# Optimization experiments

Measured on AMD Instinct MI355X. Metric: run time of the kernel, lower is better.

Reference implementation:

```python
import jax, jax.numpy as jnp
import numpy as np

B, L, E, H, W = 2, 8192, 1024, 16, 128
HD = E // H  # 64


def setup_inputs() -> dict:
    key = jax.random.key(0)
    ks = jax.random.split(key, 9)
    s = 1.0 / np.sqrt(E)
    inp = {"x": jax.random.normal(ks[0], (B, L, E), jnp.float32)}
    for i, n in enumerate(["Wq", "Wk", "Wv", "Wo"]):
        inp[n] = jax.random.uniform(ks[1 + i], (E, E), jnp.float32, -s, s)
    for i, n in enumerate(["bq", "bk", "bv", "bo"]):
        inp[n] = jax.random.uniform(ks[5 + i], (E,), jnp.float32, -s, s)
    return inp


def _skew_prob(p, w):
    # (..., w, 2w+1) -> (..., w, 3w) with row i right-shifted by i:
    # out[..., i, i+j] = p[..., i, j]  (zeros elsewhere)
    lead = p.shape[:-2]
    M, Lc = p.shape[-2], p.shape[-1]
    p = jnp.pad(p, [(0, 0)] * len(lead) + [(0, 0), (0, M + 1)])
    p = p.reshape(*lead, M * (Lc + M + 1))[..., :-M].reshape(*lead, M, M + Lc)
    return p[..., :-1]


def _sliding_attend(q, k, v, w):
    # q,k,v: (b,h,l,d); banded attention, window w on each side (2w+1 diagonals)
    b, h, l, d = q.shape
    c = l // w
    qc = q.reshape(b, h, c, w, d)
    # per-chunk key/value windows of 3w tokens (w halo each side, zero padded)
    idx = jnp.arange(c)[:, None] * w + jnp.arange(3 * w)[None, :]  # (c, 3w)
    kw = jnp.pad(k, ((0, 0), (0, 0), (w, w), (0, 0)))[:, :, idx]  # (b,h,c,3w,d)
    s = jnp.einsum('bhcqd,bhckd->bhcqk', qc, kw)  # (b,h,c,w,3w)
    # extract band: band[i, j] = s[i, i+j], j in [0, 2w] (offset d = j - w)
    gidx = (jnp.arange(w)[:, None] + jnp.arange(2 * w + 1)[None, :])[None, None, None]
    band = jnp.take_along_axis(s, gidx, axis=-1).reshape(b, h, l, 2 * w + 1)
    # mask out-of-range positions (matches the module's edge -inf loop)
    pos = jnp.arange(l)[:, None] + (jnp.arange(2 * w + 1) - w)[None, :]
    band = jnp.where((pos >= 0) & (pos < l), band, -jnp.inf)
    prob = jax.nn.softmax(band / np.sqrt(d), axis=-1)  # scale by sqrt(head_dim)
    vw = jnp.pad(v, ((0, 0), (0, 0), (w, w), (0, 0)))[:, :, idx]  # (b,h,c,3w,d)
    p3 = _skew_prob(prob.reshape(b, h, c, w, 2 * w + 1), w)  # (b,h,c,w,3w)
    ctx = jnp.einsum('bhcqk,bhckd->bhcqd', p3, vw)
    return ctx.reshape(b, h, l, d)


def reference(x, Wq, Wk, Wv, Wo, bq, bk, bv, bo):
    q = (x @ Wq.T + bq).reshape(B, L, H, HD).transpose(0, 2, 1, 3)
    k = (x @ Wk.T + bk).reshape(B, L, H, HD).transpose(0, 2, 1, 3)
    v = (x @ Wv.T + bv).reshape(B, L, H, HD).transpose(0, 2, 1, 3)
    ctx = _sliding_attend(q, k, v, W)
    ctx = ctx.transpose(0, 2, 1, 3).reshape(B, L, E)
    return ctx @ Wo.T + bo
```

## Files before the change

kernel.cpp:

```cpp
#include <hip/hip_runtime.h>
#include <math.h>

#define B_SZ  2
#define L_SEQ 8192
#define EMB   1024
#define NH    16
#define HDIM  64
#define WIN   128
#define MROWS (B_SZ*L_SEQ)

typedef __attribute__((ext_vector_type(8))) _Float16 f16x8;
typedef __attribute__((ext_vector_type(4))) _Float16 f16x4;
typedef __attribute__((ext_vector_type(4))) float f32x4;

__device__ __forceinline__ void gload16(const void* g, void* l) {
    __builtin_amdgcn_global_load_lds(
        (const __attribute__((address_space(1))) unsigned int*)g,
        (__attribute__((address_space(3))) unsigned int*)l, 16, 0, 0);
}

__global__ __launch_bounds__(256)
void round_all(const float* __restrict__ x,
               const float* __restrict__ wq, const float* __restrict__ wk,
               const float* __restrict__ wv, const float* __restrict__ wo,
               _Float16* __restrict__ xf, _Float16* __restrict__ q16,
               _Float16* __restrict__ k16, _Float16* __restrict__ v16,
               _Float16* __restrict__ o16)
{
    const size_t NX = (size_t)MROWS * EMB, NW = (size_t)EMB * EMB;
    size_t gid = ((size_t)blockIdx.x * 256 + threadIdx.x) * 4;
    const float* src; _Float16* dst; size_t off;
    if (gid < NX)               { src = x;  dst = xf;  off = gid; }
    else if (gid < NX + NW)     { src = wq; dst = q16; off = gid - NX; }
    else if (gid < NX + 2*NW)   { src = wk; dst = k16; off = gid - NX - 2*NW + NW; }
    else if (gid < NX + 3*NW)   { src = wv; dst = v16; off = gid - NX - 2*NW; }
    else                        { src = wo; dst = o16; off = gid - NX - 3*NW; }
    float4 v = *(const float4*)(src + off);
    f16x4 o;
    o[0] = (_Float16)v.x; o[1] = (_Float16)v.y;
    o[2] = (_Float16)v.z; o[3] = (_Float16)v.w;
    *(f16x4*)(dst + off) = o;
}


#define STAGE_HT(ptr_, tb_, op_, h_, kt_)                                      \
    {                                                                          \
        char* d_ = smem + (op_) * 65536 + ((kt_) & 1) * 32768 + (h_) * 16384 + ldst; \
        const _Float16* s_ = (ptr_) + ((size_t)((tb_) + (h_) * 128 + srow6)) * 1024 + (kt_) * 64 + gch; \
        gload16(s_, d_);                                                       \
        gload16(s_ + 64 * 1024, d_ + 8192);                                    \
    }

#define DSREAD_A(qr_)                                                          \
    _Pragma("unroll")                                                          \
    for (int i_ = 0; i_ < 4; ++i_) {                                           \
        const int ro_ = (qr_) * 8192 + (i_ * 16 + frow) * 128;                 \
        af[i_][0] = *(const f16x8*)(Ab + ro_ + sb0);                           \
        af[i_][1] = *(const f16x8*)(Ab + ro_ + sb1);                           \
    }

#define DSREAD_B(qc_)                                                          \
    _Pragma("unroll")                                                          \
    for (int j_ = 0; j_ < 2; ++j_) {                                           \
        const int ro_ = (brow + (qc_) * 32 + j_ * 16 + frow) * 128;            \
        bf[j_][0] = *(const f16x8*)(Bb + ro_ + sb0);                           \
        bf[j_][1] = *(const f16x8*)(Bb + ro_ + sb1);                           \
    }

#define MFMA16(qr_, qc_)                                                       \
    __builtin_amdgcn_s_setprio(1);                                             \
    _Pragma("unroll")                                                          \
    for (int ks_ = 0; ks_ < 2; ++ks_)                                          \
        _Pragma("unroll")                                                      \
        for (int i_ = 0; i_ < 4; ++i_)                                         \
            _Pragma("unroll")                                                  \
            for (int j_ = 0; j_ < 2; ++j_)                                     \
                acc[(qr_) * 4 + i_][(qc_) * 2 + j_] =                          \
                    __builtin_amdgcn_mfma_f32_16x16x32_f16(                    \
                        af[i_][ks_], bf[j_][ks_],                              \
                        acc[(qr_) * 4 + i_][(qc_) * 2 + j_], 0, 0, 0);         \
    __builtin_amdgcn_s_setprio(0);

#define BARM()                                                                 \
    asm volatile("" ::: "memory");                                             \
    __builtin_amdgcn_s_barrier();                                              \
    asm volatile("" ::: "memory");

#define GEMM8_CORE(Aptr, Bptr)                                                 \
    const int t = threadIdx.x;                                                 \
    const int wave = t >> 6, lane = t & 63;                                    \
    const int wr = wave >> 2, wc = wave & 3;                                   \
    const int frow = lane & 15, quad = lane >> 4;                              \
    const int srow6 = t >> 3;                                                  \
    const int gch = ((t & 7) ^ (srow6 & 7)) * 8;                               \
    const int ldst = t * 16;                                                   \
    const int sb0 = (quad ^ (frow & 7)) * 16, sb1 = sb0 ^ 64;                  \
    const int brow = (wc & 1) * 64;                                            \
    f32x4 acc[8][4] = {};                                                      \
    f16x8 af[4][2], bf[2][2];                                                  \
    STAGE_HT(Aptr, bm, 0, 0, 0) STAGE_HT(Aptr, bm, 0, 1, 0)                    \
    STAGE_HT(Bptr, bn, 1, 0, 0) STAGE_HT(Bptr, bn, 1, 1, 0)                    \
    for (int kt = 0; kt < 16; ++kt) {                                          \
        const char* Ab = smem + (kt & 1) * 32768 + wr * 16384;                 \
        const char* Bb = smem + 65536 + (kt & 1) * 32768 + (wc >> 1) * 16384;  \
        if (kt < 15) {                                                         \
            STAGE_HT(Aptr, bm, 0, 0, kt + 1)                                   \
            asm volatile("s_waitcnt vmcnt(2)" ::: "memory");                   \
        } else {                                                               \
            asm volatile("s_waitcnt vmcnt(0)" ::: "memory");                   \
        }                                                                      \
        BARM()                                                                 \
        DSREAD_A(0) DSREAD_B(0)                  \
        MFMA16(0, 0)                                                           \
        DSREAD_B(1)                            \
        if (kt < 15) STAGE_HT(Aptr, bm, 0, 1, kt + 1)                          \
        BARM()                                                                 \
        MFMA16(0, 1)                                                           \
        DSREAD_A(1)                                                            \
        if (kt < 15) STAGE_HT(Bptr, bn, 1, 0, kt + 1)                          \
        BARM()                                                                 \
        MFMA16(1, 1)                                                           \
        DSREAD_B(0)                                \
        if (kt < 15) STAGE_HT(Bptr, bn, 1, 1, kt + 1)                          \
        BARM()                                                                 \
        MFMA16(1, 0)                                                           \
        BARM()                                                                 \
    }

__global__ __launch_bounds__(512, 2)
void gemm_qkv(const _Float16* __restrict__ X,
              const _Float16* __restrict__ Wq, const _Float16* __restrict__ Wk,
              const _Float16* __restrict__ Wv,
              const float* __restrict__ bq, const float* __restrict__ bk,
              const float* __restrict__ bv,
              _Float16* __restrict__ qf, _Float16* __restrict__ kf,
              _Float16* __restrict__ vtf)
{
    __shared__ __attribute__((aligned(16))) char smem[131072];

    const int id = blockIdx.x;
    const int row = (id / 96) * 8 + (id & 7);
    const int colq = (id >> 3) % 12;
    const int wsel = colq >> 2;
    const int bm = row * 256, bn = (colq & 3) * 256;
    const _Float16* Bw = wsel == 0 ? Wq : wsel == 1 ? Wk : Wv;
    const float* bias = wsel == 0 ? bq : wsel == 1 ? bk : bv;
    const float scale = wsel == 0 ? 0.125f : 1.0f;

    GEMM8_CORE(X, Bw)

    char* Cw = smem + wave * 8192;
    const int bb = bm >> 13;
    const int l0 = (bm & (L_SEQ - 1)) + wr * 128;
    const int h = (bn >> 6) + wc;
    if (wsel < 2) {
        _Float16* dst = wsel == 0 ? qf : kf;
        const size_t hb = ((size_t)(bb * NH + h)) * L_SEQ * HDIM;
        #pragma unroll
        for (int ih = 0; ih < 2; ++ih) {
            asm volatile("" ::: "memory");
            #pragma unroll
            for (int i = 0; i < 4; ++i)
                #pragma unroll
                for (int j = 0; j < 4; ++j) {
                    const int lc = j * 16 + frow;
                    const float bvv = bias[bn + wc * 64 + lc];
                    #pragma unroll
                    for (int r = 0; r < 4; ++r) {
                        const int lr = i * 16 + quad * 4 + r;
                        const int bo = lr * 128 + ((lc * 2) ^ ((lr & 7) << 4));
                        *(_Float16*)(Cw + bo) = (_Float16)((acc[ih * 4 + i][j][r] + bvv) * scale);
                    }
                }
            asm volatile("" ::: "memory");
            #pragma unroll
            for (int p = 0; p < 8; ++p) {
                const int idx = p * 64 + lane;
                const int lr = idx >> 3, seg = idx & 7;
                const int bo = lr * 128 + ((seg * 16) ^ ((lr & 7) << 4));
                uint4 v = *(const uint4*)(Cw + bo);
                *(uint4*)&dst[hb + (size_t)(l0 + ih * 64 + lr) * HDIM + seg * 8] = v;
            }
        }
    } else {
        const size_t hb = ((size_t)(bb * NH + h)) * HDIM * L_SEQ;
        #pragma unroll
        for (int ih = 0; ih < 2; ++ih) {
            asm volatile("" ::: "memory");
            #pragma unroll
            for (int i = 0; i < 4; ++i)
                #pragma unroll
                for (int j = 0; j < 4; ++j) {
                    const int lc = j * 16 + frow;
                    const float bvv = bias[bn + wc * 64 + lc];
                    #pragma unroll
                    for (int r = 0; r < 4; ++r) {
                        const int lr = i * 16 + quad * 4 + r;
                        const int bo = lc * 128 + ((lr * 2) ^ ((lc & 7) << 4));
                        *(_Float16*)(Cw + bo) = (_Float16)(acc[ih * 4 + i][j][r] + bvv);
                    }
                }
            asm volatile("" ::: "memory");
            #pragma unroll
            for (int p = 0; p < 8; ++p) {
                const int idx = p * 64 + lane;
                const int dc = idx >> 3, sl = idx & 7;
                const int bo = dc * 128 + ((sl * 16) ^ ((dc & 7) << 4));
                uint4 v = *(const uint4*)(Cw + bo);
                *(uint4*)&vtf[hb + (size_t)dc * L_SEQ + (l0 + ih * 64 + sl * 8)] = v;
            }
        }
    }
}

__global__ __launch_bounds__(512, 2)
void gemm_out(const _Float16* __restrict__ A, const _Float16* __restrict__ Bwm,
              const float* __restrict__ bias, float* __restrict__ C)
{
    constexpr int N = EMB;
    __shared__ __attribute__((aligned(16))) char smem[131072];

    const int id = blockIdx.x;
    const int row = (id / 32) * 8 + (id & 7);
    const int bm = row * 256, bn = ((id >> 3) & 3) * 256;

    GEMM8_CORE(A, Bwm)

    #pragma unroll
    for (int i = 0; i < 8; ++i) {
        int m0 = bm + wr * 128 + i * 16 + quad * 4;
        #pragma unroll
        for (int j = 0; j < 4; ++j) {
            int n = bn + wc * 64 + j * 16 + frow;
            float bvv = bias[n];
            #pragma unroll
            for (int r = 0; r < 4; ++r)
                C[(size_t)(m0 + r) * N + n] = acc[i][j][r] + bvv;
        }
    }
}

__global__ __launch_bounds__(512)
void attn_mfma(const _Float16* __restrict__ qf, const _Float16* __restrict__ kf,
               const _Float16* __restrict__ vtf, _Float16* __restrict__ cf)
{
    __shared__ _Float16 Kf[2][4096], Vf[2][4096];

    const int t = threadIdx.x;
    const int wave = t >> 6, lane = t & 63;
    const int col = lane & 15, quad = lane >> 4;
    const int bh = blockIdx.y;
    const int q0 = blockIdx.x * 128;
    const int oo = wave * 16;

    f16x8 qfr[2];
    {
        size_t qidx = ((size_t)bh * L_SEQ + q0 + oo + col) * HDIM + quad * 8;
        qfr[0] = *(const f16x8*)(qf + qidx);
        qfr[1] = *(const f16x8*)(qf + qidx + 32);
    }

    f32x4 o[4] = {};
    float lsum = 0.0f;

    const int srow = t >> 3, sc = t & 7;

    const int ktlo = (q0 == 0) ? 2 : 0;
    const int kthi = (q0 == L_SEQ - 128) ? 4 : 6;

#define STAGE_KV(kt_, bsel_)                                                   \
    {                                                                          \
        const int p0s = q0 - WIN + (kt_) * 64;                                 \
        const int gq = sc ^ (srow & 7);                                        \
        size_t kgi = ((size_t)bh * L_SEQ + p0s + srow) * HDIM + gq * 8;        \
        size_t vgi = ((size_t)bh * HDIM + srow) * L_SEQ + p0s + gq * 8;        \
        gload16(kf + kgi, (char*)&Kf[bsel_][0] + t * 16);                      \
        gload16(vtf + vgi, (char*)&Vf[bsel_][0] + t * 16);                     \
    }

    STAGE_KV(ktlo, 0)

    for (int kt = ktlo; kt < kthi; kt++) {
        const int p0 = q0 - WIN + kt * 64;
        const int cb = (kt - ktlo) & 1;
        if (kt + 1 < kthi) {
            STAGE_KV(kt + 1, cb ^ 1)
            asm volatile("s_waitcnt vmcnt(2)" ::: "memory");
        } else {
            asm volatile("s_waitcnt vmcnt(0)" ::: "memory");
        }
        __builtin_amdgcn_s_barrier();
        asm volatile("" ::: "memory");

        const char* Kb = (const char*)&Kf[cb][0];
        const char* Vb = (const char*)&Vf[cb][0];

        const int relp = kt * 64 - WIN - oo;
        if (relp >= -191 && relp <= 143) {
            f32x4 sT[4] = {};
            #pragma unroll
            for (int ks = 0; ks < 2; ks++)
                #pragma unroll
                for (int n = 0; n < 4; n++) {
                    int off = (n * 16 + col) * 128 + (((ks * 4 + quad) ^ (col & 7)) * 16);
                    f16x8 kfr = *(const f16x8*)(Kb + off);
                    sT[n] = __builtin_amdgcn_mfma_f32_16x16x32_f16(kfr, qfr[ks], sT[n], 0, 0, 0);
                }
            if (relp < -113 || relp > 65) {
                const int qrow = q0 + oo + col;
                #pragma unroll
                for (int n = 0; n < 4; n++)
                    #pragma unroll
                    for (int r = 0; r < 4; r++) {
                        int dlt = (p0 + n * 16 + quad * 4 + r) - qrow;
                        if (dlt < -WIN || dlt > WIN) sT[n][r] = -3e38f;
                    }
            }
            f16x4 pT[4];
            #pragma unroll
            for (int n = 0; n < 4; n++)
                #pragma unroll
                for (int r = 0; r < 4; r++) {
                    float pv = __expf(sT[n][r]);
                    lsum += pv;
                    pT[n][r] = (_Float16)pv;
                }
            #pragma unroll
            for (int m = 0; m < 4; m++) {
                #pragma unroll
                for (int n = 0; n < 4; n++) {
                    int off = (m * 16 + col) * 128 +
                              (((2 * n + (quad >> 1)) ^ (col & 7)) * 16) + (quad & 1) * 8;
                    f16x4 vfr = *(const f16x4*)(Vb + off);
                    o[m] = __builtin_amdgcn_mfma_f32_16x16x16f16(vfr, pT[n], o[m], 0, 0, 0);
                }
            }
        }
        asm volatile("" ::: "memory");
        __builtin_amdgcn_s_barrier();
        asm volatile("" ::: "memory");
    }

    lsum += __shfl_xor(lsum, 16, 64);
    lsum += __shfl_xor(lsum, 32, 64);
    const float inv = 1.0f / lsum;

    const int b = bh >> 4, h = bh & 15;
    const size_t base = ((size_t)b * L_SEQ + q0 + oo + col) * EMB + h * HDIM;
    #pragma unroll
    for (int m = 0; m < 4; m++) {
        f16x4 ov;
        #pragma unroll
        for (int r = 0; r < 4; r++) ov[r] = (_Float16)(o[m][r] * inv);
        *(f16x4*)&cf[base + m * 16 + quad * 4] = ov;
    }
}

extern "C" void kernel_launch(void* const* d_in, const int* in_sizes, int n_in,
                              void* d_out, int out_size, void* d_ws, size_t ws_size,
                              hipStream_t stream) {
    const float* x  = (const float*)d_in[0];
    const float* Wq = (const float*)d_in[1];
    const float* Wk = (const float*)d_in[2];
    const float* Wv = (const float*)d_in[3];
    const float* Wo = (const float*)d_in[4];
    const float* bq = (const float*)d_in[5];
    const float* bk = (const float*)d_in[6];
    const float* bv = (const float*)d_in[7];
    const float* bo = (const float*)d_in[8];
    float* out = (float*)d_out;

    const size_t per = (size_t)B_SZ * NH * L_SEQ * HDIM;
    _Float16* w16 = (_Float16*)d_ws;
    _Float16* xf   = w16;
    _Float16* qf   = w16 + per;
    _Float16* kf   = w16 + 2 * per;
    _Float16* vtf  = w16 + 3 * per;
    _Float16* cf   = w16 + 4 * per;
    _Float16* wq16 = w16 + 5 * per;
    _Float16* wk16 = wq16 + 1048576;
    _Float16* wv16 = wq16 + 2 * 1048576;
    _Float16* wo16 = wq16 + 3 * 1048576;

    const int nround = (MROWS * EMB + 4 * EMB * EMB) / 1024;
    round_all<<<nround, dim3(256), 0, stream>>>(x, Wq, Wk, Wv, Wo, xf, wq16, wk16, wv16, wo16);

    gemm_qkv<<<768, dim3(512), 0, stream>>>(xf, wq16, wk16, wv16, bq, bk, bv, qf, kf, vtf);

    attn_mfma<<<dim3(L_SEQ / 128, B_SZ * NH), dim3(512), 0, stream>>>(qf, kf, vtf, cf);

    gemm_out<<<256, dim3(512), 0, stream>>>(cf, wo16, bo, out);
}
```

Before: 314.3 us.

## Restructure GEMM mainloop into unrolled double-buffered phases with deeper prefetch

```diff
diff --git a/kernel.cpp b/kernel.cpp
--- a/kernel.cpp
+++ b/kernel.cpp
@@ -51,20 +51,20 @@
         gload16(s_ + 64 * 1024, d_ + 8192);                                    \
     }
 
-#define DSREAD_A(qr_)                                                          \
+#define DSR_A(base_, qr_)                                                      \
     _Pragma("unroll")                                                          \
     for (int i_ = 0; i_ < 4; ++i_) {                                           \
-        const int ro_ = (qr_) * 8192 + (i_ * 16 + frow) * 128;                 \
-        af[i_][0] = *(const f16x8*)(Ab + ro_ + sb0);                           \
-        af[i_][1] = *(const f16x8*)(Ab + ro_ + sb1);                           \
-    }
-
-#define DSREAD_B(qc_)                                                          \
+        const int ro_ = ((qr_) * 64 + i_ * 16 + frow) * 128;                   \
+        af[i_][0] = *(const f16x8*)((base_) + ro_ + sb0);                      \
+        af[i_][1] = *(const f16x8*)((base_) + ro_ + sb1);                      \
+    }
+
+#define DSR_B(base_, qc_)                                                      \
     _Pragma("unroll")                                                          \
     for (int j_ = 0; j_ < 2; ++j_) {                                           \
         const int ro_ = (brow + (qc_) * 32 + j_ * 16 + frow) * 128;            \
-        bf[j_][0] = *(const f16x8*)(Bb + ro_ + sb0);                           \
-        bf[j_][1] = *(const f16x8*)(Bb + ro_ + sb1);                           \
+        bf[j_][0] = *(const f16x8*)((base_) + ro_ + sb0);                      \
+        bf[j_][1] = *(const f16x8*)((base_) + ro_ + sb1);                      \
     }
 
 #define MFMA16(qr_, qc_)                                                       \
@@ -86,6 +86,19 @@
     __builtin_amdgcn_s_barrier();                                              \
     asm volatile("" ::: "memory");
 
+#define VW4 asm volatile("s_waitcnt vmcnt(4)" ::: "memory");
+#define VW0 asm volatile("s_waitcnt vmcnt(0)" ::: "memory");
+#define NOST
+#define NOWT
+
+#define PHASE(RD_, ST_, WT_, mq_, nq_)                                         \
+    RD_                                                                        \
+    ST_                                                                        \
+    WT_                                                                        \
+    BARM()                                                                     \
+    MFMA16(mq_, nq_)                                                           \
+    BARM()
+
 #define GEMM8_CORE(Aptr, Bptr)                                                 \
     const int t = threadIdx.x;                                                 \
     const int wave = t >> 6, lane = t & 63;                                    \
@@ -96,36 +109,37 @@
     const int ldst = t * 16;                                                   \
     const int sb0 = (quad ^ (frow & 7)) * 16, sb1 = sb0 ^ 64;                  \
     const int brow = (wc & 1) * 64;                                            \
+    const char* Ab0 = smem + wr * 16384;                                       \
+    const char* Ab1 = smem + 32768 + wr * 16384;                               \
+    const char* Bb0 = smem + 65536 + (wc >> 1) * 16384;                        \
+    const char* Bb1 = smem + 98304 + (wc >> 1) * 16384;                        \
     f32x4 acc[8][4] = {};                                                      \
     f16x8 af[4][2], bf[2][2];                                                  \
     STAGE_HT(Aptr, bm, 0, 0, 0) STAGE_HT(Aptr, bm, 0, 1, 0)                    \
     STAGE_HT(Bptr, bn, 1, 0, 0) STAGE_HT(Bptr, bn, 1, 1, 0)                    \
-    for (int kt = 0; kt < 16; ++kt) {                                          \
-        const char* Ab = smem + (kt & 1) * 32768 + wr * 16384;                 \
-        const char* Bb = smem + 65536 + (kt & 1) * 32768 + (wc >> 1) * 16384;  \
-        if (kt < 15) {                                                         \
-            STAGE_HT(Aptr, bm, 0, 0, kt + 1)                                   \
-            asm volatile("s_waitcnt vmcnt(2)" ::: "memory");                   \
-        } else {                                                               \
-            asm volatile("s_waitcnt vmcnt(0)" ::: "memory");                   \
-        }                                                                      \
-        BARM()                                                                 \
-        DSREAD_A(0) DSREAD_B(0)                  \
-        MFMA16(0, 0)                                                           \
-        DSREAD_B(1)                            \
-        if (kt < 15) STAGE_HT(Aptr, bm, 0, 1, kt + 1)                          \
-        BARM()                                                                 \
-        MFMA16(0, 1)                                                           \
-        DSREAD_A(1)                                                            \
-        if (kt < 15) STAGE_HT(Bptr, bn, 1, 0, kt + 1)                          \
-        BARM()                                                                 \
-        MFMA16(1, 1)                                                           \
-        DSREAD_B(0)                                \
-        if (kt < 15) STAGE_HT(Bptr, bn, 1, 1, kt + 1)                          \
-        BARM()                                                                 \
-        MFMA16(1, 0)                                                           \
-        BARM()                                                                 \
-    }
+    STAGE_HT(Aptr, bm, 0, 0, 1)                                                \
+    asm volatile("s_waitcnt vmcnt(2)" ::: "memory");                           \
+    BARM()                                                                     \
+    for (int it = 0; it < 7; ++it) {                                           \
+        const int kb = it * 2;                                                 \
+        PHASE(DSR_A(Ab0,0) DSR_B(Bb0,0), STAGE_HT(Aptr,bm,0,1,kb+1), VW4, 0,0) \
+        PHASE(DSR_B(Bb0,1),              STAGE_HT(Bptr,bn,1,0,kb+1), VW4, 0,1) \
+        PHASE(DSR_A(Ab0,1),              STAGE_HT(Bptr,bn,1,1,kb+1), VW4, 1,1) \
+        PHASE(DSR_B(Bb0,0),              STAGE_HT(Aptr,bm,0,0,kb+2), VW4, 1,0) \
+        PHASE(DSR_A(Ab1,0) DSR_B(Bb1,0), STAGE_HT(Aptr,bm,0,1,kb+2), VW4, 0,0) \
+        PHASE(DSR_B(Bb1,1),              STAGE_HT(Bptr,bn,1,0,kb+2), VW4, 0,1) \
+        PHASE(DSR_A(Ab1,1),              STAGE_HT(Bptr,bn,1,1,kb+2), VW4, 1,1) \
+        PHASE(DSR_B(Bb1,0),              STAGE_HT(Aptr,bm,0,0,kb+3), VW4, 1,0) \
+    }                                                                          \
+                \
+    PHASE(DSR_A(Ab0,0) DSR_B(Bb0,0), STAGE_HT(Aptr,bm,0,1,15), VW4, 0,0)       \
+    PHASE(DSR_B(Bb0,1),              STAGE_HT(Bptr,bn,1,0,15), VW4, 0,1)       \
+    PHASE(DSR_A(Ab0,1),              STAGE_HT(Bptr,bn,1,1,15), VW4, 1,1)       \
+    PHASE(DSR_B(Bb0,0),              NOST,                     VW0, 1,0)       \
+    PHASE(DSR_A(Ab1,0) DSR_B(Bb1,0), NOST,                     NOWT, 0,0)      \
+    PHASE(DSR_B(Bb1,1),              NOST,                     NOWT, 0,1)      \
+    PHASE(DSR_A(Ab1,1),              NOST,                     NOWT, 1,1)      \
+    PHASE(DSR_B(Bb1,0),              NOST,                     NOWT, 1,0)
 
 __global__ __launch_bounds__(512, 2)
 void gemm_qkv(const _Float16* __restrict__ X,
```

New measurement: 326.9 us. 4.0% more time.
